# Optimization experiments

Measured on AMD Instinct MI355X. Metric: run time of the kernel, lower is better.

The kernel has to match this reference:

```python
import jax, jax.numpy as jnp
import numpy as np

# mcorrlcorr hyperparameters (closed over as constants; int args to the op)
S = (1, 2)   # stride (sx, sy)
D = (1, 1)   # dilation (dx, dy)
P = (0, 2)   # padding (px, py)
U = (1, 1)   # upsample / input dilation (ux, uy)
R = (0, 0)   # extra output size (rx, ry)


def _out_sizes(nfx, nfy, ngx, ngy):
    sx, sy = S; dx, dy = D; px, py = P; ux, uy = U; rx, ry = R
    # mcorr_valid_size along x, lcorr_valid_size along y (from source)
    nhx = max((ngx + ux - 1) * (px + 1) // (nfx + dx - 1) - sx + 1, 0) + rx
    nhy = max((uy * (ngy - 1) - dy * (nfy - 1) + py) // sy + 1, 0) + ry
    return nhx, nhy


def setup_inputs() -> dict:
    key = jax.random.key(0)
    k1, k2, k3 = jax.random.split(key, 3)
    input = jax.random.normal(k1, (16, 32, 128, 384), dtype=jnp.float32)
    weight = jax.random.normal(k2, (64, 32, 4, 8), dtype=jnp.float32) * 0.05
    bias = jax.random.normal(k3, (64,), dtype=jnp.float32) * 0.05
    return {"input": input, "weight": weight, "bias": bias}


def _mcorrlcorr(input, weight, bias):
    batch, c_in, ngx, ngy = input.shape
    c_out, _, nfx, nfy = weight.shape
    sx, sy = S; dx, dy = D; px, py = P; ux, uy = U
    nhx, nhy = _out_sizes(nfx, nfy, ngx, ngy)
    px1 = px + 1

    # --- multiplicative (Mellin) correlation along x ---
    # gx = (hx+sx)*(fx+dx)/(px+1) - ux  when divisible and in [0, ngx)
    hx = jnp.arange(nhx)
    fxi = jnp.arange(nfx)
    num_x = (hx[:, None] + sx) * (fxi[None, :] + dx)          # [nhx, nfx]
    gx = num_x // px1 - ux
    vx = (num_x % px1 == 0) & (gx >= 0) & (gx < ngx)
    gxc = jnp.clip(gx, 0, ngx - 1)
    # gather along x: G1[b, c, hx, fx, gy_full]
    G1 = input[:, :, gxc, :] * vx.astype(input.dtype)[None, None, :, :, None]

    # contract channels and fx, keep fy separate: U[b, o, hx, fy, ngy]
    Ufy = jnp.einsum('bcxfg,ocfy->boxyg', G1, weight)

    # --- linear correlation along y ---
    # gy = (sy*hy - py + dy*fy)/uy  when divisible and in [0, ngy)
    hy = jnp.arange(nhy)
    fyi = jnp.arange(nfy)
    num_y = sy * hy[:, None] - py + dy * fyi[None, :]          # [nhy, nfy]
    gy = num_y // uy
    vy = (num_y % uy == 0) & (gy >= 0) & (gy < ngy)
    gyc = jnp.clip(gy, 0, ngy - 1)

    def gather_fy(Uf, gyf, vyf):
        # Uf: [b, o, nhx, ngy]; gyf, vyf: [nhy]
        return Uf[..., gyf] * vyf.astype(Uf.dtype)

    # vmap over fy axis (axis 3 of Ufy, axis 1 of gyc/vy) -> [nfy, b, o, nhx, nhy]
    per_fy = jax.vmap(gather_fy, in_axes=(3, 1, 1), out_axes=0)(Ufy, gyc, vy)
    h = per_fy.sum(0) + bias[None, :, None, None]
    return h


def reference(input, weight, bias):
    return _mcorrlcorr(input, weight, bias)
```

## Files before the change

kernel.cpp:

```cpp
#include <hip/hip_runtime.h>
#include <hip/hip_bf16.h>


#define Bb   16
#define NGX  128
#define NGY  384
#define Oo   64
#define NHX  32
#define NHY  190

#define HEAD 4
#define RSX  400
#define XBUF (16 * RSX)

typedef short bf16x8 __attribute__((ext_vector_type(8)));
typedef float f32x4  __attribute__((ext_vector_type(4)));
typedef unsigned short u16x4 __attribute__((ext_vector_type(4)));

__device__ __forceinline__ unsigned short f2bf(float f) {
  __hip_bfloat16 h = __float2bfloat16(f);
  return __builtin_bit_cast(unsigned short, h);
}

__global__ void wprep_kernel(const float* __restrict__ w, unsigned short* __restrict__ wl) {
  int idx = blockIdx.x * 256 + threadIdx.x;
  if (idx >= Oo * 1024) return;
  int k8 = idx >> 9;
  int o  = (idx >> 3) & 63;
  int j  = idx & 7;
  wl[idx] = f2bf(w[o * 1024 + k8 * 8 + j]);
}

__global__ __launch_bounds__(512, 4)
void mcorr_mfma_kernel(const float* __restrict__ in, const unsigned short* __restrict__ wl,
                       const float* __restrict__ bias, float* __restrict__ out) {
  const int tid  = threadIdx.x;
  const int l    = tid & 63;
  const int wv   = tid >> 6;
  const int wo   = wv >> 2;
  const int whq  = wv & 3;
  const int lo16 = l & 15, gq = l >> 4;

  int lid = blockIdx.x + NHX * blockIdx.y;
  int swz = (lid & 7) * 64 + (lid >> 3);
  const int hx = swz & 31;
  const int b  = swz >> 5;

  __shared__ __align__(16) unsigned short xs_[2 * XBUF];

  f32x4 acc[2][3];
  #pragma unroll
  for (int i = 0; i < 2; ++i)
    #pragma unroll
    for (int j = 0; j < 3; ++j) acc[i][j] = (f32x4){0.f, 0.f, 0.f, 0.f};

  {
    int bu = tid >> 8, row = (tid >> 4) & 15, j = tid & 15;
    xs_[bu * XBUF + row * RSX + (j < HEAD ? j : 384 + j)] = 0;
  }

  const int r_st  = tid >> 5;
  const int j0    = tid & 31;
  const int fx_st = r_st & 3;
  const int c_st  = r_st >> 2;
  const int gx_st = (hx + 1) * (fx_st + 1) - 1;
  const float* xbase = in + (((size_t)b * 32 + c_st) * NGX + gx_st) * NGY;
  const size_t cstep = (size_t)4 * NGX * NGY;

  float4 xv[2][3];

#define XLOAD(T) do {                                                    \
    const float* xb_ = xbase + (size_t)(T) * cstep;                      \
    _Pragma("unroll") for (int s_ = 0; s_ < 3; ++s_)                     \
      xv[(T) & 1][s_] = *(const float4*)(xb_ + 4 * j0 + 128 * s_);       \
  } while (0)

#define XCOMMIT(T) do {                                                  \
    unsigned short* row_ = xs_ + ((T) & 1) * XBUF + r_st * RSX;          \
    _Pragma("unroll") for (int s_ = 0; s_ < 3; ++s_) {                   \
      u16x4 h_;                                                          \
      h_[0] = f2bf(xv[(T) & 1][s_].x); h_[1] = f2bf(xv[(T) & 1][s_].y);  \
      h_[2] = f2bf(xv[(T) & 1][s_].z); h_[3] = f2bf(xv[(T) & 1][s_].w);  \
      *(u16x4*)&row_[HEAD + 4 * j0 + 128 * s_] = h_;                     \
    }                                                                    \
  } while (0)

#define BAR() do {                                                       \
    asm volatile("s_waitcnt lgkmcnt(0)" ::: "memory");                   \
    __builtin_amdgcn_s_barrier();                                        \
  } while (0)

#define COMPUTE(T) do {                                                              \
    const unsigned* Xb_ = (const unsigned*)(xs_ + ((T) & 1) * XBUF);                 \
    _Pragma("unroll") for (int cs_ = 0; cs_ < 4; ++cs_) {                            \
      const unsigned short* ap_ =                                                    \
          wl + ((4 * (T) + cs_) * 4 + gq) * 512 + (32 * wo + lo16) * 8;              \
      bf16x8 a0_ = *(const bf16x8*)ap_;                                              \
      bf16x8 a1_ = *(const bf16x8*)(ap_ + 128);                           \
      const int r_ = cs_ * 4 + gq;                                                   \
      _Pragma("unroll") for (int tt_ = 0; tt_ < 3; ++tt_) {                          \
        int hy_ = 48 * whq + 16 * tt_ + lo16;                                        \
        const unsigned* xp_ = &Xb_[r_ * 200 + 1 + hy_];                              \
        union { unsigned u[4]; bf16x8 v; } bb_;                                      \
        bb_.u[0] = xp_[0]; bb_.u[1] = xp_[1];                                        \
        bb_.u[2] = xp_[2]; bb_.u[3] = xp_[3];                                        \
        acc[0][tt_] = __builtin_amdgcn_mfma_f32_16x16x32_bf16(                       \
            a0_, bb_.v, acc[0][tt_], 0, 0, 0);                                       \
        acc[1][tt_] = __builtin_amdgcn_mfma_f32_16x16x32_bf16(                       \
            a1_, bb_.v, acc[1][tt_], 0, 0, 0);                                       \
      }                                                                              \
    }                                                                                \
  } while (0)

  XLOAD(0);
  XLOAD(1);
  XCOMMIT(0);
  BAR();

  #pragma unroll
  for (int t = 0; t < 8; ++t) {
    if (t < 6) XLOAD(t + 2);
    COMPUTE(t);
    if (t < 7) { XCOMMIT(t + 1); BAR(); }
  }

  #pragma unroll
  for (int mt = 0; mt < 2; ++mt) {
    #pragma unroll
    for (int reg = 0; reg < 4; ++reg) {
      int o = 32 * wo + 16 * mt + 4 * gq + reg;
      float bv = bias[o];
      #pragma unroll
      for (int tt = 0; tt < 3; ++tt) {
        int hy = 48 * whq + 16 * tt + lo16;
        if (hy < NHY)
          out[(((size_t)b * Oo + o) * NHX + hx) * NHY + hy] = acc[mt][tt][reg] + bv;
      }
    }
  }
}

extern "C" void kernel_launch(void* const* d_in, const int* in_sizes, int n_in,
                              void* d_out, int out_size, void* d_ws, size_t ws_size,
                              hipStream_t stream) {
  const float* in   = (const float*)d_in[0];
  const float* w    = (const float*)d_in[1];
  const float* bias = (const float*)d_in[2];
  float* out = (float*)d_out;
  unsigned short* wl = (unsigned short*)d_ws;

  wprep_kernel<<<(Oo * 1024 + 255) / 256, 256, 0, stream>>>(w, wl);

  dim3 grid(NHX, Bb);
  mcorr_mfma_kernel<<<grid, 512, 0, stream>>>(in, wl, bias, out);
}
```

Before: 32.72 us.

## Split output hy range across two blocks to double grid and halve LDS

Each block now computes half of the hy output range (95 columns), giving 1024 blocks instead of 512. The LDS row buffer shrinks to about half, and each wave handles 16 output channels instead of 32, so per-thread accumulators are halved. Launch bounds are raised to allow 8 blocks per CU. The aim is better occupancy and load balance across CUs. The cost is that the overlapping halo of input rows is loaded twice and each weight fragment is reused over fewer MFMAs.

```diff
diff --git a/kernel.cpp b/kernel.cpp
--- a/kernel.cpp
+++ b/kernel.cpp
@@ -8,9 +8,10 @@
 #define Oo   64
 #define NHX  32
 #define NHY  190
+#define NHYH 95
 
-#define HEAD 4
-#define RSX  400
+#define RDW  104
+#define RSX  (2 * RDW)
 #define XBUF (16 * RSX)
 
 typedef short bf16x8 __attribute__((ext_vector_type(8)));
@@ -31,32 +32,31 @@
   wl[idx] = f2bf(w[o * 1024 + k8 * 8 + j]);
 }
 
-__global__ __launch_bounds__(512, 4)
+__global__ __launch_bounds__(512, 8)
 void mcorr_mfma_kernel(const float* __restrict__ in, const unsigned short* __restrict__ wl,
                        const float* __restrict__ bias, float* __restrict__ out) {
   const int tid  = threadIdx.x;
   const int l    = tid & 63;
   const int wv   = tid >> 6;
-  const int wo   = wv >> 2;
-  const int whq  = wv & 3;
+  const int wo   = wv & 3;
+  const int whq  = wv >> 2;
   const int lo16 = l & 15, gq = l >> 4;
 
-  int lid = blockIdx.x + NHX * blockIdx.y;
-  int swz = (lid & 7) * 64 + (lid >> 3);
-  const int hx = swz & 31;
-  const int b  = swz >> 5;
+  int lid = blockIdx.x;
+  int swz = (lid & 7) * 128 + (lid >> 3);
+  const int b  = swz >> 6;
+  const int hx = (swz >> 1) & 31;
+  const int h  = swz & 1;
 
   __shared__ __align__(16) unsigned short xs_[2 * XBUF];
 
-  f32x4 acc[2][3];
+  f32x4 acc[3];
   #pragma unroll
-  for (int i = 0; i < 2; ++i)
-    #pragma unroll
-    for (int j = 0; j < 3; ++j) acc[i][j] = (f32x4){0.f, 0.f, 0.f, 0.f};
+  for (int j = 0; j < 3; ++j) acc[j] = (f32x4){0.f, 0.f, 0.f, 0.f};
 
-  {
-    int bu = tid >> 8, row = (tid >> 4) & 15, j = tid & 15;
-    xs_[bu * XBUF + row * RSX + (j < HEAD ? j : 384 + j)] = 0;
+  if (tid < 2 * 16 * 12) {
+    int bu = tid / 192, rem = tid % 192, row = rem / 12, j = rem % 12;
+    xs_[bu * XBUF + row * RSX + (j < 4 ? j : 196 + j)] = 0;
   }
 
   const int r_st  = tid >> 5;
@@ -64,24 +64,29 @@
   const int fx_st = r_st & 3;
   const int c_st  = r_st >> 2;
   const int gx_st = (hx + 1) * (fx_st + 1) - 1;
-  const float* xbase = in + (((size_t)b * 32 + c_st) * NGX + gx_st) * NGY;
+  const int Gs    = 188 * h;
+  const float* xbase = in + (((size_t)b * 32 + c_st) * NGX + gx_st) * NGY + Gs;
   const size_t cstep = (size_t)4 * NGX * NGY;
+  const int D0 = 1 + h;
 
-  float4 xv[2][3];
+  float4 xv[2][2];
 
 #define XLOAD(T) do {                                                    \
     const float* xb_ = xbase + (size_t)(T) * cstep;                      \
-    _Pragma("unroll") for (int s_ = 0; s_ < 3; ++s_)                     \
-      xv[(T) & 1][s_] = *(const float4*)(xb_ + 4 * j0 + 128 * s_);       \
+    xv[(T) & 1][0] = *(const float4*)(xb_ + 4 * j0);                     \
+    if (j0 < 17) xv[(T) & 1][1] = *(const float4*)(xb_ + 128 + 4 * j0);  \
   } while (0)
 
 #define XCOMMIT(T) do {                                                  \
     unsigned short* row_ = xs_ + ((T) & 1) * XBUF + r_st * RSX;          \
-    _Pragma("unroll") for (int s_ = 0; s_ < 3; ++s_) {                   \
-      u16x4 h_;                                                          \
-      h_[0] = f2bf(xv[(T) & 1][s_].x); h_[1] = f2bf(xv[(T) & 1][s_].y);  \
-      h_[2] = f2bf(xv[(T) & 1][s_].z); h_[3] = f2bf(xv[(T) & 1][s_].w);  \
-      *(u16x4*)&row_[HEAD + 4 * j0 + 128 * s_] = h_;                     \
+    _Pragma("unroll") for (int s_ = 0; s_ < 2; ++s_) {                   \
+      if (s_ == 0 || j0 < 17) {                                          \
+        float4 v_ = xv[(T) & 1][s_];                                     \
+        u16x4 h_;                                                        \
+        h_[0] = f2bf(v_.x); h_[1] = f2bf(v_.y);                          \
+        h_[2] = f2bf(v_.z); h_[3] = f2bf(v_.w);                          \
+        *(u16x4*)&row_[4 + 4 * j0 + 128 * s_] = h_;                      \
+      }                                                                  \
     }                                                                    \
   } while (0)
 
@@ -94,20 +99,17 @@
     const unsigned* Xb_ = (const unsigned*)(xs_ + ((T) & 1) * XBUF);                 \
     _Pragma("unroll") for (int cs_ = 0; cs_ < 4; ++cs_) {                            \
       const unsigned short* ap_ =                                                    \
-          wl + ((4 * (T) + cs_) * 4 + gq) * 512 + (32 * wo + lo16) * 8;              \
-      bf16x8 a0_ = *(const bf16x8*)ap_;                                              \
-      bf16x8 a1_ = *(const bf16x8*)(ap_ + 128);                           \
+          wl + ((4 * (T) + cs_) * 4 + gq) * 512 + (16 * wo + lo16) * 8;              \
+      bf16x8 a_ = *(const bf16x8*)ap_;                                               \
       const int r_ = cs_ * 4 + gq;                                                   \
       _Pragma("unroll") for (int tt_ = 0; tt_ < 3; ++tt_) {                          \
         int hy_ = 48 * whq + 16 * tt_ + lo16;                                        \
-        const unsigned* xp_ = &Xb_[r_ * 200 + 1 + hy_];                              \
+        const unsigned* xp_ = &Xb_[r_ * RDW + D0 + hy_];                             \
         union { unsigned u[4]; bf16x8 v; } bb_;                                      \
         bb_.u[0] = xp_[0]; bb_.u[1] = xp_[1];                                        \
         bb_.u[2] = xp_[2]; bb_.u[3] = xp_[3];                                        \
-        acc[0][tt_] = __builtin_amdgcn_mfma_f32_16x16x32_bf16(                       \
-            a0_, bb_.v, acc[0][tt_], 0, 0, 0);                                       \
-        acc[1][tt_] = __builtin_amdgcn_mfma_f32_16x16x32_bf16(                       \
-            a1_, bb_.v, acc[1][tt_], 0, 0, 0);                                       \
+        acc[tt_] = __builtin_amdgcn_mfma_f32_16x16x32_bf16(                          \
+            a_, bb_.v, acc[tt_], 0, 0, 0);                                           \
       }                                                                              \
     }                                                                                \
   } while (0)
@@ -125,17 +127,14 @@
   }
 
   #pragma unroll
-  for (int mt = 0; mt < 2; ++mt) {
+  for (int reg = 0; reg < 4; ++reg) {
+    int o = 16 * wo + 4 * gq + reg;
+    float bv = bias[o];
     #pragma unroll
-    for (int reg = 0; reg < 4; ++reg) {
-      int o = 32 * wo + 16 * mt + 4 * gq + reg;
-      float bv = bias[o];
-      #pragma unroll
-      for (int tt = 0; tt < 3; ++tt) {
-        int hy = 48 * whq + 16 * tt + lo16;
-        if (hy < NHY)
-          out[(((size_t)b * Oo + o) * NHX + hx) * NHY + hy] = acc[mt][tt][reg] + bv;
-      }
+    for (int tt = 0; tt < 3; ++tt) {
+      int hyl = 48 * whq + 16 * tt + lo16;
+      if (hyl < NHYH)
+        out[(((size_t)b * Oo + o) * NHX + hx) * NHY + NHYH * h + hyl] = acc[tt][reg] + bv;
     }
   }
 }
@@ -151,6 +150,5 @@
 
   wprep_kernel<<<(Oo * 1024 + 255) / 256, 256, 0, stream>>>(w, wl);
 
-  dim3 grid(NHX, Bb);
-  mcorr_mfma_kernel<<<grid, 512, 0, stream>>>(in, wl, bias, out);
+  mcorr_mfma_kernel<<<1024, 512, 0, stream>>>(in, wl, bias, out);
 }
```

Result: slower. 40.66 us (+24.3%).

## Stage bf16 weight tiles into LDS via async global_load_lds double buffering

Applied to the files above, without the earlier changes.

Weight fragments, which each wave previously read straight from global memory inside the MFMA loop, are now copied per channel-tile into a double-buffered LDS region using global_load_lds. The copy for the next tile is issued ahead of compute and overlapped with it. Explicit vmcnt waits and sched_barriers order these copies against the input loads. This adds 32KB of LDS per block, which may reduce occupancy, and the vmcnt accounting must stay exact.

```diff
diff --git a/kernel.cpp b/kernel.cpp
--- a/kernel.cpp
+++ b/kernel.cpp
@@ -12,6 +12,7 @@
 #define HEAD 4
 #define RSX  400
 #define XBUF (16 * RSX)
+#define ATIL 8192
 
 typedef short bf16x8 __attribute__((ext_vector_type(8)));
 typedef float f32x4  __attribute__((ext_vector_type(4)));
@@ -24,7 +25,6 @@
 
 __global__ void wprep_kernel(const float* __restrict__ w, unsigned short* __restrict__ wl) {
   int idx = blockIdx.x * 256 + threadIdx.x;
-  if (idx >= Oo * 1024) return;
   int k8 = idx >> 9;
   int o  = (idx >> 3) & 63;
   int j  = idx & 7;
@@ -46,7 +46,9 @@
   const int hx = swz & 31;
   const int b  = swz >> 5;
 
-  __shared__ __align__(16) unsigned short xs_[2 * XBUF];
+  __shared__ __align__(16) unsigned short smem[2 * ATIL + 2 * XBUF];
+  unsigned short* As_ = smem;
+  unsigned short* xs_ = smem + 2 * ATIL;
 
   f32x4 acc[2][3];
   #pragma unroll
@@ -68,6 +70,16 @@
   const size_t cstep = (size_t)4 * NGX * NGY;
 
   float4 xv[2][3];
+
+#define AISSUE(T) do {                                                   \
+    _Pragma("unroll") for (int r_ = 0; r_ < 2; ++r_)                     \
+      __builtin_amdgcn_global_load_lds(                                  \
+          (const __attribute__((address_space(1))) void*)                \
+              (wl + (size_t)(T) * ATIL + r_ * 4096 + tid * 8),           \
+          (__attribute__((address_space(3))) void*)                      \
+              (As_ + ((T) & 1) * ATIL + r_ * 4096 + tid * 8),            \
+          16, 0, 0);                                                     \
+  } while (0)
 
 #define XLOAD(T) do {                                                    \
     const float* xb_ = xbase + (size_t)(T) * cstep;                      \
@@ -91,10 +103,11 @@
   } while (0)
 
 #define COMPUTE(T) do {                                                              \
+    const unsigned short* Ab_ = As_ + ((T) & 1) * ATIL;                              \
     const unsigned* Xb_ = (const unsigned*)(xs_ + ((T) & 1) * XBUF);                 \
     _Pragma("unroll") for (int cs_ = 0; cs_ < 4; ++cs_) {                            \
       const unsigned short* ap_ =                                                    \
-          wl + ((4 * (T) + cs_) * 4 + gq) * 512 + (32 * wo + lo16) * 8;              \
+          Ab_ + (4 * cs_ + gq) * 512 + (32 * wo + lo16) * 8;                         \
       bf16x8 a0_ = *(const bf16x8*)ap_;                                              \
       bf16x8 a1_ = *(const bf16x8*)(ap_ + 128);                           \
       const int r_ = cs_ * 4 + gq;                                                   \
@@ -112,16 +125,28 @@
     }                                                                                \
   } while (0)
 
+  AISSUE(0);
   XLOAD(0);
   XLOAD(1);
   XCOMMIT(0);
+  __builtin_amdgcn_sched_barrier(0);
+  asm volatile("s_waitcnt vmcnt(3)" ::: "memory");
   BAR();
 
   #pragma unroll
   for (int t = 0; t < 8; ++t) {
+    if (t < 7) AISSUE(t + 1);
+    __builtin_amdgcn_sched_barrier(0);
     if (t < 6) XLOAD(t + 2);
+    __builtin_amdgcn_sched_barrier(0);
     COMPUTE(t);
-    if (t < 7) { XCOMMIT(t + 1); BAR(); }
+    if (t < 7) {
+      XCOMMIT(t + 1);
+      __builtin_amdgcn_sched_barrier(0);
+      if (t < 6) asm volatile("s_waitcnt vmcnt(3)" ::: "memory");
+      else       asm volatile("s_waitcnt vmcnt(0)" ::: "memory");
+      BAR();
+    }
   }
 
   #pragma unroll
@@ -149,7 +174,7 @@
   float* out = (float*)d_out;
   unsigned short* wl = (unsigned short*)d_ws;
 
-  wprep_kernel<<<(Oo * 1024 + 255) / 256, 256, 0, stream>>>(w, wl);
+  wprep_kernel<<<Oo * 1024 / 256, 256, 0, stream>>>(w, wl);
 
   dim3 grid(NHX, Bb);
   mcorr_mfma_kernel<<<grid, 512, 0, stream>>>(in, wl, bias, out);
```

Measured after the change: 33.36 us. About the same (+2.0%).

## Fuse weight bf16 conversion into main kernel via double-buffered LDS tiles

Applied to the files above, without the earlier changes.

Drops the separate weight-prep kernel launch. Each block now loads fp32 weights per K-step, converts them to bf16 and stages them in a double-buffered, XOR-swizzled LDS tile, and MFMA operands are read from LDS instead of global memory. A sched_barrier is added to keep the global loads ahead of the compute. This saves one launch and the workspace round trip, but every block now repeats the weight conversion, and the larger LDS footprint may lower occupancy.

```diff
diff --git a/kernel.cpp b/kernel.cpp
--- a/kernel.cpp
+++ b/kernel.cpp
@@ -12,6 +12,7 @@
 #define HEAD 4
 #define RSX  400
 #define XBUF (16 * RSX)
+#define ATIL 8192
 
 typedef short bf16x8 __attribute__((ext_vector_type(8)));
 typedef float f32x4  __attribute__((ext_vector_type(4)));
@@ -22,17 +23,8 @@
   return __builtin_bit_cast(unsigned short, h);
 }
 
-__global__ void wprep_kernel(const float* __restrict__ w, unsigned short* __restrict__ wl) {
-  int idx = blockIdx.x * 256 + threadIdx.x;
-  if (idx >= Oo * 1024) return;
-  int k8 = idx >> 9;
-  int o  = (idx >> 3) & 63;
-  int j  = idx & 7;
-  wl[idx] = f2bf(w[o * 1024 + k8 * 8 + j]);
-}
-
 __global__ __launch_bounds__(512, 4)
-void mcorr_mfma_kernel(const float* __restrict__ in, const unsigned short* __restrict__ wl,
+void mcorr_mfma_kernel(const float* __restrict__ in, const float* __restrict__ w,
                        const float* __restrict__ bias, float* __restrict__ out) {
   const int tid  = threadIdx.x;
   const int l    = tid & 63;
@@ -40,13 +32,17 @@
   const int wo   = wv >> 2;
   const int whq  = wv & 3;
   const int lo16 = l & 15, gq = l >> 4;
+  const int l5   = tid & 31;
+  const int og   = tid >> 5;
 
   int lid = blockIdx.x + NHX * blockIdx.y;
   int swz = (lid & 7) * 64 + (lid >> 3);
   const int hx = swz & 31;
   const int b  = swz >> 5;
 
-  __shared__ __align__(16) unsigned short xs_[2 * XBUF];
+  __shared__ __align__(16) unsigned short smem[2 * ATIL + 2 * XBUF];
+  unsigned short* As_ = smem;
+  unsigned short* xs_ = smem + 2 * ATIL;
 
   f32x4 acc[2][3];
   #pragma unroll
@@ -60,7 +56,6 @@
   }
 
   const int r_st  = tid >> 5;
-  const int j0    = tid & 31;
   const int fx_st = r_st & 3;
   const int c_st  = r_st >> 2;
   const int gx_st = (hx + 1) * (fx_st + 1) - 1;
@@ -68,11 +63,30 @@
   const size_t cstep = (size_t)4 * NGX * NGY;
 
   float4 xv[2][3];
+  float4 av[4];
+
+#define ALOAD(T) do {                                                    \
+    _Pragma("unroll") for (int r_ = 0; r_ < 4; ++r_)                     \
+      av[r_] = *(const float4*)(w + (size_t)(16 * r_ + og) * 1024 +      \
+                                128 * (T) + 4 * l5);                     \
+  } while (0)
+
+#define ACOMMIT(T) do {                                                  \
+    unsigned short* Ad_ = As_ + ((T) & 1) * ATIL;                        \
+    const int gl_ = l5 >> 1;                                             \
+    _Pragma("unroll") for (int r_ = 0; r_ < 4; ++r_) {                   \
+      int op_ = (16 * r_ + og) ^ (gl_ & 7);                              \
+      u16x4 h_;                                                          \
+      h_[0] = f2bf(av[r_].x); h_[1] = f2bf(av[r_].y);                    \
+      h_[2] = f2bf(av[r_].z); h_[3] = f2bf(av[r_].w);                    \
+      *(u16x4*)&Ad_[gl_ * 512 + op_ * 8 + 4 * (l5 & 1)] = h_;            \
+    }                                                                    \
+  } while (0)
 
 #define XLOAD(T) do {                                                    \
     const float* xb_ = xbase + (size_t)(T) * cstep;                      \
     _Pragma("unroll") for (int s_ = 0; s_ < 3; ++s_)                     \
-      xv[(T) & 1][s_] = *(const float4*)(xb_ + 4 * j0 + 128 * s_);       \
+      xv[(T) & 1][s_] = *(const float4*)(xb_ + 4 * l5 + 128 * s_);       \
   } while (0)
 
 #define XCOMMIT(T) do {                                                  \
@@ -81,7 +95,7 @@
       u16x4 h_;                                                          \
       h_[0] = f2bf(xv[(T) & 1][s_].x); h_[1] = f2bf(xv[(T) & 1][s_].y);  \
       h_[2] = f2bf(xv[(T) & 1][s_].z); h_[3] = f2bf(xv[(T) & 1][s_].w);  \
-      *(u16x4*)&row_[HEAD + 4 * j0 + 128 * s_] = h_;                     \
+      *(u16x4*)&row_[HEAD + 4 * l5 + 128 * s_] = h_;                     \
     }                                                                    \
   } while (0)
 
@@ -91,12 +105,14 @@
   } while (0)
 
 #define COMPUTE(T) do {                                                              \
+    const unsigned short* Ab_ = As_ + ((T) & 1) * ATIL;                              \
     const unsigned* Xb_ = (const unsigned*)(xs_ + ((T) & 1) * XBUF);                 \
     _Pragma("unroll") for (int cs_ = 0; cs_ < 4; ++cs_) {                            \
+      const int gl_ = 4 * cs_ + gq;                                                  \
       const unsigned short* ap_ =                                                    \
-          wl + ((4 * (T) + cs_) * 4 + gq) * 512 + (32 * wo + lo16) * 8;              \
+          Ab_ + gl_ * 512 + ((32 * wo + lo16) ^ (gl_ & 7)) * 8;                      \
       bf16x8 a0_ = *(const bf16x8*)ap_;                                              \
-      bf16x8 a1_ = *(const bf16x8*)(ap_ + 128);                           \
+      bf16x8 a1_ = *(const bf16x8*)(ap_ + 128);          \
       const int r_ = cs_ * 4 + gq;                                                   \
       _Pragma("unroll") for (int tt_ = 0; tt_ < 3; ++tt_) {                          \
         int hy_ = 48 * whq + 16 * tt_ + lo16;                                        \
@@ -112,16 +128,24 @@
     }                                                                                \
   } while (0)
 
+  ALOAD(0);
   XLOAD(0);
   XLOAD(1);
+  ACOMMIT(0);
   XCOMMIT(0);
   BAR();
 
   #pragma unroll
   for (int t = 0; t < 8; ++t) {
+    if (t < 7) ALOAD(t + 1);
     if (t < 6) XLOAD(t + 2);
+    __builtin_amdgcn_sched_barrier(0);
     COMPUTE(t);
-    if (t < 7) { XCOMMIT(t + 1); BAR(); }
+    if (t < 7) {
+      ACOMMIT(t + 1);
+      XCOMMIT(t + 1);
+      BAR();
+    }
   }
 
   #pragma unroll
@@ -147,10 +171,7 @@
   const float* w    = (const float*)d_in[1];
   const float* bias = (const float*)d_in[2];
   float* out = (float*)d_out;
-  unsigned short* wl = (unsigned short*)d_ws;
-
-  wprep_kernel<<<(Oo * 1024 + 255) / 256, 256, 0, stream>>>(w, wl);
 
   dim3 grid(NHX, Bb);
-  mcorr_mfma_kernel<<<grid, 512, 0, stream>>>(in, wl, bias, out);
+  mcorr_mfma_kernel<<<grid, 512, 0, stream>>>(in, w, bias, out);
 }
```

After: 43.78 us. +33.8%, slower.
